# Kernel optimization log

Hardware: AMD Instinct MI355X
Metric: run time of the kernel (lower is better)

The kernel has to match this reference:

```python
import jax, jax.numpy as jnp
import numpy as np

LOG_STD2 = float(np.log(0.001))  # matches nn.init posterior_W_u/v fill, unused: params are random here


def _mvg_layer(x, M, u, v, eps):
    # append ones column (bias trick): [B, in] -> [B, in+1]
    x1 = jnp.concatenate([x, jnp.ones((x.shape[0], 1), x.dtype)], axis=1)
    # W = M + diag(exp(.5u)) @ eps @ diag(exp(.5v))  ==  M + row/col scaled eps
    W = M + jnp.exp(0.5 * u)[:, None] * eps * jnp.exp(0.5 * v)[None, :]
    return x1 @ W


def setup_inputs() -> dict:
    key = jax.random.key(0)
    ks = jax.random.split(key, 17)
    dims = [(2049, 4096), (4097, 4096), (4097, 4096), (4097, 2048)]
    inp = {"x": jax.random.normal(ks[0], (8192, 2048), dtype=jnp.float32)}
    ki = 1
    for i, (fin, fout) in enumerate(dims):
        inp[f"M{i}"] = jax.random.normal(ks[ki], (fin, fout), dtype=jnp.float32) * 0.001; ki += 1
        inp[f"u{i}"] = jax.random.normal(ks[ki], (fin,), dtype=jnp.float32) + LOG_STD2; ki += 1
        inp[f"v{i}"] = jax.random.normal(ks[ki], (fout,), dtype=jnp.float32) + LOG_STD2; ki += 1
        inp[f"eps{i}"] = jax.random.normal(ks[ki], (fin, fout), dtype=jnp.float32); ki += 1
    return inp


def reference(x, M0, u0, v0, eps0, M1, u1, v1, eps1, M2, u2, v2, eps2, M3, u3, v3, eps3):
    h = _mvg_layer(x, M0, u0, v0, eps0)
    h = _mvg_layer(jax.nn.relu(h), M1, u1, v1, eps1)
    h = _mvg_layer(jax.nn.relu(h), M2, u2, v2, eps2)
    h = _mvg_layer(jax.nn.relu(h), M3, u3, v3, eps3)
    return h
```

## Files before the change

### kernel.cpp

```cpp
#include <hip/hip_runtime.h>
#include <cstdint>
#include <cstddef>

typedef __bf16 bf16_t;
typedef __attribute__((ext_vector_type(8))) __bf16 bf16x8;
typedef __attribute__((ext_vector_type(4))) __bf16 bf16x4;
typedef __attribute__((ext_vector_type(4))) float floatx4;

#define SB0 __builtin_amdgcn_sched_barrier(0)
#define LGKM(N)                                             \
  do {                                                      \
    asm volatile("s_waitcnt lgkmcnt(" #N ")" ::: "memory"); \
    SB0;                                                    \
  } while (0)

__device__ __forceinline__ void cp16(const void* g, void* l) {
  __builtin_amdgcn_global_load_lds(
      (const __attribute__((address_space(1))) void*)(uintptr_t)g,
      (__attribute__((address_space(3))) void*)(uintptr_t)l, 16, 0, 0);
}

__device__ __forceinline__ void stage_half(const bf16_t* p, int K, char* dst,
                                           int tid) {
  cp16(p, dst + tid * 16);
  cp16(p + (size_t)128 * K, dst + 8192 + tid * 16);
}

struct PrepArgs {
  const float* x;
  bf16_t* xb;
  const float* M[4];
  const float* u[4];
  const float* v[4];
  const float* e[4];
  bf16_t* Wt[4];
  float* bias[4];
};

__global__ __launch_bounds__(256) void prep_all(PrepArgs a) {
  __shared__ float tile[32][33];
  const int tx = threadIdx.x, ty = threadIdx.y;
  const int tid = ty * 32 + tx;
  int bid = blockIdx.x;

  if (bid < 16384) {
    const int i = bid * 256 + tid;
    float4 f = ((const float4*)a.x)[i];
    bf16x4 o;
    o[0] = (bf16_t)f.x; o[1] = (bf16_t)f.y; o[2] = (bf16_t)f.z; o[3] = (bf16_t)f.w;
    ((bf16x4*)a.xb)[i] = o;
    return;
  }
  bid -= 16384;

  if (bid >= 49152) {
    const int b = bid - 49152;
    int layer, base;
    if (b < 16) { layer = 0; base = b; }
    else if (b < 32) { layer = 1; base = b - 16; }
    else if (b < 48) { layer = 2; base = b - 32; }
    else { layer = 3; base = b - 48; }
    const int K = (layer == 0) ? 2048 : 4096;
    const int N = (layer == 3) ? 2048 : 4096;
    const int n = base * 256 + tid;
    if (n < N) {
      const size_t idx = (size_t)K * N + n;
      a.bias[layer][n] = a.M[layer][idx] +
                         __expf(0.5f * a.u[layer][K]) * a.e[layer][idx] *
                             __expf(0.5f * a.v[layer][n]);
    }
    return;
  }

  int layer, nbx, kby, K, N;
  if (bid < 8192) { layer = 0; K = 2048; N = 4096; nbx = bid & 127; kby = bid >> 7; }
  else if (bid < 24576) { layer = 1; K = 4096; N = 4096; int b = bid - 8192; nbx = b & 127; kby = b >> 7; }
  else if (bid < 40960) { layer = 2; K = 4096; N = 4096; int b = bid - 24576; nbx = b & 127; kby = b >> 7; }
  else { layer = 3; K = 4096; N = 2048; int b = bid - 40960; nbx = b & 63; kby = b >> 6; }
  const float* M = a.M[layer];
  const float* u = a.u[layer];
  const float* v = a.v[layer];
  const float* eps = a.e[layer];
  bf16_t* Wt = a.Wt[layer];
  const int nb = nbx * 32, kb = kby * 32;
  const float sv = __expf(0.5f * v[nb + tx]);
#pragma unroll
  for (int r = 0; r < 4; ++r) {
    const int k = kb + ty + 8 * r;
    const float su = __expf(0.5f * u[k]);
    const size_t idx = (size_t)k * N + nb + tx;
    tile[ty + 8 * r][tx] = M[idx] + su * eps[idx] * sv;
  }
  __syncthreads();
#pragma unroll
  for (int r = 0; r < 4; ++r) {
    const int n = nb + ty + 8 * r;
    Wt[(size_t)n * K + kb + tx] = (bf16_t)tile[tx][ty + 8 * r];
  }
}

__device__ __forceinline__ void half16(const char* Ah, const char* Bh, int aoff,
                                       int boff, floatx4 (&acc)[8][4]) {
  bf16x8 af[8], bb[4];
  af[0] = *(const bf16x8*)(Ah + aoff);
  bb[0] = *(const bf16x8*)(Bh + boff);
  bb[1] = *(const bf16x8*)(Bh + boff + 1024);
  bb[2] = *(const bf16x8*)(Bh + boff + 2048);
  bb[3] = *(const bf16x8*)(Bh + boff + 3072);
  SB0;
  af[1] = *(const bf16x8*)(Ah + aoff + 1024);
  SB0;
  af[2] = *(const bf16x8*)(Ah + aoff + 2048);
  SB0;
  af[3] = *(const bf16x8*)(Ah + aoff + 3072);
  SB0;
  af[4] = *(const bf16x8*)(Ah + aoff + 4096);
  SB0;
  af[5] = *(const bf16x8*)(Ah + aoff + 5120);
  SB0;
  af[6] = *(const bf16x8*)(Ah + aoff + 6144);
  SB0;
  af[7] = *(const bf16x8*)(Ah + aoff + 7168);
  SB0;
  __builtin_amdgcn_s_setprio(1);
  LGKM(7);
#pragma unroll
  for (int j = 0; j < 4; ++j)
    acc[0][j] = __builtin_amdgcn_mfma_f32_16x16x32_bf16(bb[j], af[0], acc[0][j], 0, 0, 0);
  LGKM(6);
#pragma unroll
  for (int j = 0; j < 4; ++j)
    acc[1][j] = __builtin_amdgcn_mfma_f32_16x16x32_bf16(bb[j], af[1], acc[1][j], 0, 0, 0);
  LGKM(5);
#pragma unroll
  for (int j = 0; j < 4; ++j)
    acc[2][j] = __builtin_amdgcn_mfma_f32_16x16x32_bf16(bb[j], af[2], acc[2][j], 0, 0, 0);
  LGKM(4);
#pragma unroll
  for (int j = 0; j < 4; ++j)
    acc[3][j] = __builtin_amdgcn_mfma_f32_16x16x32_bf16(bb[j], af[3], acc[3][j], 0, 0, 0);
  LGKM(3);
#pragma unroll
  for (int j = 0; j < 4; ++j)
    acc[4][j] = __builtin_amdgcn_mfma_f32_16x16x32_bf16(bb[j], af[4], acc[4][j], 0, 0, 0);
  LGKM(2);
#pragma unroll
  for (int j = 0; j < 4; ++j)
    acc[5][j] = __builtin_amdgcn_mfma_f32_16x16x32_bf16(bb[j], af[5], acc[5][j], 0, 0, 0);
  LGKM(1);
#pragma unroll
  for (int j = 0; j < 4; ++j)
    acc[6][j] = __builtin_amdgcn_mfma_f32_16x16x32_bf16(bb[j], af[6], acc[6][j], 0, 0, 0);
  LGKM(0);
#pragma unroll
  for (int j = 0; j < 4; ++j)
    acc[7][j] = __builtin_amdgcn_mfma_f32_16x16x32_bf16(bb[j], af[7], acc[7][j], 0, 0, 0);
  __builtin_amdgcn_s_setprio(0);
}

template <int CURB>
__device__ __forceinline__ void ktile(int t, int NT, int K, const bf16_t* gA,
                                      const bf16_t* gB, char* lds, int tid,
                                      int aoff0, int boff0, int firstO,
                                      floatx4 (&acc)[8][4]) {
  constexpr int curO = CURB * 65536;
  constexpr int nxtO = (CURB ^ 1) * 65536;
  if (t + 1 < NT) {
    const bf16_t* pa = gA + (size_t)(t + 1) * 64;
    const bf16_t* pb = gB + (size_t)(t + 1) * 64;
    stage_half(pa, K, lds + nxtO, tid);
    stage_half(pa + 32, K, lds + nxtO + 16384, tid);
    stage_half(pb, K, lds + nxtO + 32768, tid);
    stage_half(pb + 32, K, lds + nxtO + 49152, tid);
  }
  SB0;
  const int h0 = firstO;
  const int h1 = 16384 - firstO;
  half16(lds + curO + h0, lds + curO + 32768 + h0, aoff0, boff0, acc);
  half16(lds + curO + h1, lds + curO + 32768 + h1, aoff0, boff0, acc);
  if (t + 1 < NT) {
    asm volatile("s_waitcnt vmcnt(0)" ::: "memory");
  }
  SB0;
  __builtin_amdgcn_s_barrier();
  SB0;
}

template <int EPI>
__global__ __launch_bounds__(512, 2) void gemm256(
    const bf16_t* __restrict__ A, const bf16_t* __restrict__ Bt,
    const float* __restrict__ bias, void* __restrict__ Cout, int N, int K) {
  extern __shared__ char lds[];
  const int tid = threadIdx.x;
  const int lane = tid & 63;
  const int wave = tid >> 6;
  const int wm = (wave >> 2) * 128;
  const int wn = (wave & 3) * 64;
  const int l15 = lane & 15;
  const int kqs = ((lane >> 4) ^ ((lane >> 1) & 3)) << 4;
  const int aoff0 = (wm + l15) * 64 + kqs;
  const int boff0 = (wn + l15) * 64 + kqs;
  const int firstO = (wave < 4) ? 0 : 16384;

  const int gx = gridDim.x;
  int id = blockIdx.y * gx + blockIdx.x;
  const int cpx = (gx * (int)gridDim.y) >> 3;
  id = (id & 7) * cpx + (id >> 3);
  const int bm = (id / gx) * 256;
  const int bn = (id % gx) * 256;

  const int srow = tid >> 2;
  const int ss8 = ((tid & 3) ^ ((tid >> 3) & 3)) * 8;
  const bf16_t* gA = A + (size_t)(bm + srow) * K + ss8;
  const bf16_t* gB = Bt + (size_t)(bn + srow) * K + ss8;

  const int NT = K >> 6;

  floatx4 acc[8][4] = {};

  stage_half(gA, K, lds + 0, tid);
  stage_half(gA + 32, K, lds + 16384, tid);
  stage_half(gB, K, lds + 32768, tid);
  stage_half(gB + 32, K, lds + 49152, tid);
  asm volatile("s_waitcnt vmcnt(0)" ::: "memory");
  __builtin_amdgcn_s_barrier();
  SB0;

  for (int t = 0; t < NT; t += 2) {
    ktile<0>(t, NT, K, gA, gB, lds, tid, aoff0, boff0, firstO, acc);
    ktile<1>(t + 1, NT, K, gA, gB, lds, tid, aoff0, boff0, firstO, acc);
  }

  const int kq4 = lane >> 4;
  const int row00 = bm + wm + l15;
  const int colq = bn + wn + kq4 * 4;
  float4 b4[4];
#pragma unroll
  for (int j = 0; j < 4; ++j) b4[j] = *(const float4*)&bias[colq + j * 16];
#pragma unroll
  for (int i = 0; i < 8; ++i) {
    const size_t rbase = (size_t)(row00 + i * 16) * N;
#pragma unroll
    for (int j = 0; j < 4; ++j) {
      float x0 = acc[i][j][0] + b4[j].x;
      float x1 = acc[i][j][1] + b4[j].y;
      float x2 = acc[i][j][2] + b4[j].z;
      float x3 = acc[i][j][3] + b4[j].w;
      if (EPI == 0) {
        x0 = fmaxf(x0, 0.f);
        x1 = fmaxf(x1, 0.f);
        x2 = fmaxf(x2, 0.f);
        x3 = fmaxf(x3, 0.f);
        bf16x4 o;
        o[0] = (bf16_t)x0; o[1] = (bf16_t)x1; o[2] = (bf16_t)x2; o[3] = (bf16_t)x3;
        *(bf16x4*)((bf16_t*)Cout + rbase + colq + j * 16) = o;
      } else {
        float4 o = make_float4(x0, x1, x2, x3);
        *(float4*)((float*)Cout + rbase + colq + j * 16) = o;
      }
    }
  }
}

extern "C" void kernel_launch(void* const* d_in, const int* in_sizes, int n_in,
                              void* d_out, int out_size, void* d_ws, size_t ws_size,
                              hipStream_t stream) {
  const float* x = (const float*)d_in[0];
  const float *Mm[4], *uu[4], *vv[4], *ee[4];
  for (int i = 0; i < 4; ++i) {
    Mm[i] = (const float*)d_in[1 + 4 * i];
    uu[i] = (const float*)d_in[2 + 4 * i];
    vv[i] = (const float*)d_in[3 + 4 * i];
    ee[i] = (const float*)d_in[4 + 4 * i];
  }

  char* ws = (char*)d_ws;
  bf16_t* Wt0 = (bf16_t*)ws;
  bf16_t* Wt1 = (bf16_t*)(ws + 16777216);
  bf16_t* Wt2 = (bf16_t*)(ws + 16777216 + 33554432);
  bf16_t* Wt3 = (bf16_t*)(ws + 16777216 + 2u * 33554432);
  char* bptr = ws + 2u * 16777216 + 2u * 33554432;
  float* bias0 = (float*)(bptr);
  float* bias1 = (float*)(bptr + 16384);
  float* bias2 = (float*)(bptr + 32768);
  float* bias3 = (float*)(bptr + 49152);
  char* act = bptr + 65536;
  bf16_t* hA = (bf16_t*)act;
  bf16_t* hB = (bf16_t*)(act + 67108864);
  bf16_t* xb = (bf16_t*)d_out;

  static bool attr_set = false;
  if (!attr_set) {
    (void)hipFuncSetAttribute(reinterpret_cast<const void*>(&gemm256<0>),
                              hipFuncAttributeMaxDynamicSharedMemorySize, 131072);
    (void)hipFuncSetAttribute(reinterpret_cast<const void*>(&gemm256<1>),
                              hipFuncAttributeMaxDynamicSharedMemorySize, 131072);
    attr_set = true;
  }

  PrepArgs pa;
  pa.x = x;
  pa.xb = xb;
  for (int i = 0; i < 4; ++i) {
    pa.M[i] = Mm[i]; pa.u[i] = uu[i]; pa.v[i] = vv[i]; pa.e[i] = ee[i];
  }
  pa.Wt[0] = Wt0; pa.Wt[1] = Wt1; pa.Wt[2] = Wt2; pa.Wt[3] = Wt3;
  pa.bias[0] = bias0; pa.bias[1] = bias1; pa.bias[2] = bias2; pa.bias[3] = bias3;
  prep_all<<<16384 + 49152 + 56, dim3(32, 8), 0, stream>>>(pa);

  gemm256<0><<<dim3(16, 32), 512, 131072, stream>>>(xb, Wt0, bias0, hA, 4096, 2048);
  gemm256<0><<<dim3(16, 32), 512, 131072, stream>>>(hA, Wt1, bias1, hB, 4096, 4096);
  gemm256<0><<<dim3(16, 32), 512, 131072, stream>>>(hB, Wt2, bias2, hA, 4096, 4096);
  gemm256<1><<<dim3(8, 32), 512, 131072, stream>>>(hA, Wt3, bias3, d_out, 2048, 4096);
}
```

Before: 1.326 ms.

## Interleave LDS fragment loads and split-half global prefetch with MFMA in GEMM k-tile

Restructures the GEMM inner k-tile so LDS fragment reads for the second k-half are issued between MFMAs of the first half, instead of being loaded up front per half. Global-to-LDS staging is split into halves: the second k-half of the next tile and the first k-half of the tile after next are issued at different points. A mid-tile barrier lets the current buffer's first half be refilled early. The aim is to hide LDS and global latency behind matrix math and avoid a full vmcnt(0) drain each iteration. In exchange the waitcnt and barrier ordering is intricate, and a mistake in it could cause races or stalls.

```diff
diff --git a/kernel.cpp b/kernel.cpp
--- a/kernel.cpp
+++ b/kernel.cpp
@@ -13,6 +13,8 @@
     asm volatile("s_waitcnt lgkmcnt(" #N ")" ::: "memory"); \
     SB0;                                                    \
   } while (0)
+#define MM(i, j, A, B) \
+  acc[i][j] = __builtin_amdgcn_mfma_f32_16x16x32_bf16(B, A, acc[i][j], 0, 0, 0)
 
 __device__ __forceinline__ void cp16(const void* g, void* l) {
   __builtin_amdgcn_global_load_lds(
@@ -99,86 +101,107 @@
   }
 }
 
-__device__ __forceinline__ void half16(const char* Ah, const char* Bh, int aoff,
-                                       int boff, floatx4 (&acc)[8][4]) {
-  bf16x8 af[8], bb[4];
-  af[0] = *(const bf16x8*)(Ah + aoff);
-  bb[0] = *(const bf16x8*)(Bh + boff);
-  bb[1] = *(const bf16x8*)(Bh + boff + 1024);
-  bb[2] = *(const bf16x8*)(Bh + boff + 2048);
-  bb[3] = *(const bf16x8*)(Bh + boff + 3072);
-  SB0;
-  af[1] = *(const bf16x8*)(Ah + aoff + 1024);
-  SB0;
-  af[2] = *(const bf16x8*)(Ah + aoff + 2048);
-  SB0;
-  af[3] = *(const bf16x8*)(Ah + aoff + 3072);
-  SB0;
-  af[4] = *(const bf16x8*)(Ah + aoff + 4096);
-  SB0;
-  af[5] = *(const bf16x8*)(Ah + aoff + 5120);
-  SB0;
-  af[6] = *(const bf16x8*)(Ah + aoff + 6144);
-  SB0;
-  af[7] = *(const bf16x8*)(Ah + aoff + 7168);
-  SB0;
-  __builtin_amdgcn_s_setprio(1);
-  LGKM(7);
-#pragma unroll
-  for (int j = 0; j < 4; ++j)
-    acc[0][j] = __builtin_amdgcn_mfma_f32_16x16x32_bf16(bb[j], af[0], acc[0][j], 0, 0, 0);
-  LGKM(6);
-#pragma unroll
-  for (int j = 0; j < 4; ++j)
-    acc[1][j] = __builtin_amdgcn_mfma_f32_16x16x32_bf16(bb[j], af[1], acc[1][j], 0, 0, 0);
-  LGKM(5);
-#pragma unroll
-  for (int j = 0; j < 4; ++j)
-    acc[2][j] = __builtin_amdgcn_mfma_f32_16x16x32_bf16(bb[j], af[2], acc[2][j], 0, 0, 0);
-  LGKM(4);
-#pragma unroll
-  for (int j = 0; j < 4; ++j)
-    acc[3][j] = __builtin_amdgcn_mfma_f32_16x16x32_bf16(bb[j], af[3], acc[3][j], 0, 0, 0);
-  LGKM(3);
-#pragma unroll
-  for (int j = 0; j < 4; ++j)
-    acc[4][j] = __builtin_amdgcn_mfma_f32_16x16x32_bf16(bb[j], af[4], acc[4][j], 0, 0, 0);
-  LGKM(2);
-#pragma unroll
-  for (int j = 0; j < 4; ++j)
-    acc[5][j] = __builtin_amdgcn_mfma_f32_16x16x32_bf16(bb[j], af[5], acc[5][j], 0, 0, 0);
-  LGKM(1);
-#pragma unroll
-  for (int j = 0; j < 4; ++j)
-    acc[6][j] = __builtin_amdgcn_mfma_f32_16x16x32_bf16(bb[j], af[6], acc[6][j], 0, 0, 0);
-  LGKM(0);
-#pragma unroll
-  for (int j = 0; j < 4; ++j)
-    acc[7][j] = __builtin_amdgcn_mfma_f32_16x16x32_bf16(bb[j], af[7], acc[7][j], 0, 0, 0);
-  __builtin_amdgcn_s_setprio(0);
-}
-
 template <int CURB>
 __device__ __forceinline__ void ktile(int t, int NT, int K, const bf16_t* gA,
                                       const bf16_t* gB, char* lds, int tid,
-                                      int aoff0, int boff0, int firstO,
-                                      floatx4 (&acc)[8][4]) {
+                                      int aoff0, int boff0, floatx4 (&acc)[8][4]) {
   constexpr int curO = CURB * 65536;
   constexpr int nxtO = (CURB ^ 1) * 65536;
-  if (t + 1 < NT) {
-    const bf16_t* pa = gA + (size_t)(t + 1) * 64;
-    const bf16_t* pb = gB + (size_t)(t + 1) * 64;
-    stage_half(pa, K, lds + nxtO, tid);
-    stage_half(pa + 32, K, lds + nxtO + 16384, tid);
-    stage_half(pb, K, lds + nxtO + 32768, tid);
-    stage_half(pb + 32, K, lds + nxtO + 49152, tid);
-  }
-  SB0;
-  const int h0 = firstO;
-  const int h1 = 16384 - firstO;
-  half16(lds + curO + h0, lds + curO + 32768 + h0, aoff0, boff0, acc);
-  half16(lds + curO + h1, lds + curO + 32768 + h1, aoff0, boff0, acc);
-  if (t + 1 < NT) {
+  const char* Ab0 = lds + curO + aoff0;
+  const char* Ab1 = lds + curO + 16384 + aoff0;
+  const char* Bb0 = lds + curO + 32768 + boff0;
+  const char* Bb1 = lds + curO + 49152 + boff0;
+  bf16x8 afA[4], afB[4], afC[4], bbX[4], bbY[4];
+
+  afA[0] = *(const bf16x8*)(Ab0);
+  afA[1] = *(const bf16x8*)(Ab0 + 1024);
+  afA[2] = *(const bf16x8*)(Ab0 + 2048);
+  afA[3] = *(const bf16x8*)(Ab0 + 3072);
+  bbX[0] = *(const bf16x8*)(Bb0);
+  bbX[1] = *(const bf16x8*)(Bb0 + 1024);
+  bbX[2] = *(const bf16x8*)(Bb0 + 2048);
+  bbX[3] = *(const bf16x8*)(Bb0 + 3072);
+  SB0;
+  afB[0] = *(const bf16x8*)(Ab0 + 4096);
+  afB[1] = *(const bf16x8*)(Ab0 + 5120);
+  afB[2] = *(const bf16x8*)(Ab0 + 6144);
+  afB[3] = *(const bf16x8*)(Ab0 + 7168);
+  SB0;
+  if (t + 1 < NT)
+    stage_half(gA + (size_t)(t + 1) * 64 + 32, K, lds + nxtO + 16384, tid);
+  SB0;
+  LGKM(4);
+  __builtin_amdgcn_s_setprio(1);
+  MM(0, 0, afA[0], bbX[0]); MM(0, 1, afA[0], bbX[1]);
+  afC[0] = *(const bf16x8*)(Ab1); SB0;
+  MM(0, 2, afA[0], bbX[2]); MM(0, 3, afA[0], bbX[3]);
+  afC[1] = *(const bf16x8*)(Ab1 + 1024); SB0;
+  MM(1, 0, afA[1], bbX[0]); MM(1, 1, afA[1], bbX[1]);
+  afC[2] = *(const bf16x8*)(Ab1 + 2048); SB0;
+  MM(1, 2, afA[1], bbX[2]); MM(1, 3, afA[1], bbX[3]);
+  afC[3] = *(const bf16x8*)(Ab1 + 3072); SB0;
+  MM(2, 0, afA[2], bbX[0]); MM(2, 1, afA[2], bbX[1]);
+  bbY[0] = *(const bf16x8*)(Bb1); SB0;
+  MM(2, 2, afA[2], bbX[2]); MM(2, 3, afA[2], bbX[3]);
+  bbY[1] = *(const bf16x8*)(Bb1 + 1024); SB0;
+  MM(3, 0, afA[3], bbX[0]); MM(3, 1, afA[3], bbX[1]);
+  bbY[2] = *(const bf16x8*)(Bb1 + 2048); SB0;
+  MM(3, 2, afA[3], bbX[2]); MM(3, 3, afA[3], bbX[3]);
+  bbY[3] = *(const bf16x8*)(Bb1 + 3072);
+  if (t + 1 < NT)
+    stage_half(gB + (size_t)(t + 1) * 64 + 32, K, lds + nxtO + 49152, tid);
+  SB0;
+  LGKM(8);
+  MM(4, 0, afB[0], bbX[0]); MM(4, 1, afB[0], bbX[1]);
+  MM(4, 2, afB[0], bbX[2]); MM(4, 3, afB[0], bbX[3]);
+  afA[0] = *(const bf16x8*)(Ab1 + 4096); SB0;
+  MM(5, 0, afB[1], bbX[0]); MM(5, 1, afB[1], bbX[1]);
+  MM(5, 2, afB[1], bbX[2]); MM(5, 3, afB[1], bbX[3]);
+  afA[1] = *(const bf16x8*)(Ab1 + 5120); SB0;
+  MM(6, 0, afB[2], bbX[0]); MM(6, 1, afB[2], bbX[1]);
+  MM(6, 2, afB[2], bbX[2]); MM(6, 3, afB[2], bbX[3]);
+  afA[2] = *(const bf16x8*)(Ab1 + 6144); SB0;
+  MM(7, 0, afB[3], bbX[0]); MM(7, 1, afB[3], bbX[1]);
+  MM(7, 2, afB[3], bbX[2]); MM(7, 3, afB[3], bbX[3]);
+  afA[3] = *(const bf16x8*)(Ab1 + 7168); SB0;
+  __builtin_amdgcn_s_setprio(0);
+  SB0;
+  __builtin_amdgcn_s_barrier();
+  SB0;
+  LGKM(4);
+  __builtin_amdgcn_s_setprio(1);
+  MM(0, 0, afC[0], bbY[0]); MM(0, 1, afC[0], bbY[1]);
+  MM(0, 2, afC[0], bbY[2]); MM(0, 3, afC[0], bbY[3]);
+  SB0;
+  if (t + 2 < NT)
+    stage_half(gA + (size_t)(t + 2) * 64, K, lds + curO, tid);
+  SB0;
+  MM(1, 0, afC[1], bbY[0]); MM(1, 1, afC[1], bbY[1]);
+  MM(1, 2, afC[1], bbY[2]); MM(1, 3, afC[1], bbY[3]);
+  SB0;
+  if (t + 2 < NT)
+    stage_half(gB + (size_t)(t + 2) * 64, K, lds + curO + 32768, tid);
+  SB0;
+  MM(2, 0, afC[2], bbY[0]); MM(2, 1, afC[2], bbY[1]);
+  MM(2, 2, afC[2], bbY[2]); MM(2, 3, afC[2], bbY[3]);
+  SB0;
+  MM(3, 0, afC[3], bbY[0]); MM(3, 1, afC[3], bbY[1]);
+  MM(3, 2, afC[3], bbY[2]); MM(3, 3, afC[3], bbY[3]);
+  SB0;
+  LGKM(0);
+  MM(4, 0, afA[0], bbY[0]); MM(4, 1, afA[0], bbY[1]);
+  MM(4, 2, afA[0], bbY[2]); MM(4, 3, afA[0], bbY[3]);
+  MM(5, 0, afA[1], bbY[0]); MM(5, 1, afA[1], bbY[1]);
+  MM(5, 2, afA[1], bbY[2]); MM(5, 3, afA[1], bbY[3]);
+  MM(6, 0, afA[2], bbY[0]); MM(6, 1, afA[2], bbY[1]);
+  MM(6, 2, afA[2], bbY[2]); MM(6, 3, afA[2], bbY[3]);
+  MM(7, 0, afA[3], bbY[0]); MM(7, 1, afA[3], bbY[1]);
+  MM(7, 2, afA[3], bbY[2]); MM(7, 3, afA[3], bbY[3]);
+  __builtin_amdgcn_s_setprio(0);
+  SB0;
+  if (t + 2 < NT) {
+    asm volatile("s_waitcnt vmcnt(4)" ::: "memory");
+  } else if (t + 1 < NT) {
     asm volatile("s_waitcnt vmcnt(0)" ::: "memory");
   }
   SB0;
@@ -200,7 +223,6 @@
   const int kqs = ((lane >> 4) ^ ((lane >> 1) & 3)) << 4;
   const int aoff0 = (wm + l15) * 64 + kqs;
   const int boff0 = (wn + l15) * 64 + kqs;
-  const int firstO = (wave < 4) ? 0 : 16384;
 
   const int gx = gridDim.x;
   int id = blockIdx.y * gx + blockIdx.x;
@@ -222,13 +244,15 @@
   stage_half(gA + 32, K, lds + 16384, tid);
   stage_half(gB, K, lds + 32768, tid);
   stage_half(gB + 32, K, lds + 49152, tid);
-  asm volatile("s_waitcnt vmcnt(0)" ::: "memory");
+  stage_half(gA + 64, K, lds + 65536, tid);
+  stage_half(gB + 64, K, lds + 65536 + 32768, tid);
+  asm volatile("s_waitcnt vmcnt(4)" ::: "memory");
   __builtin_amdgcn_s_barrier();
   SB0;
 
   for (int t = 0; t < NT; t += 2) {
-    ktile<0>(t, NT, K, gA, gB, lds, tid, aoff0, boff0, firstO, acc);
-    ktile<1>(t + 1, NT, K, gA, gB, lds, tid, aoff0, boff0, firstO, acc);
+    ktile<0>(t, NT, K, gA, gB, lds, tid, aoff0, boff0, acc);
+    ktile<1>(t + 1, NT, K, gA, gB, lds, tid, aoff0, boff0, acc);
   }
 
   const int kq4 = lane >> 4;
```

Result: slower. 1.708 ms (+28.8%).
